# Performance work log

Measured on AMD Instinct MI355X. Metric: run time of the kernel, lower is better.

## Reference

```python
import jax, jax.numpy as jnp
import numpy as np

DIM, HEADS, EMB = 768, 16, 1024
DH = DIM // HEADS                 # 48, divisible by 3 for 3D RoPE
T, RES = 3, 24
KT, KH, KW = 3, 5, 5              # neighborhood kernel
MLP = 4 * DIM
EPS = 1e-5


def _ln(x, w=None, b=None):
    m = x.mean(-1, keepdims=True)
    v = x.var(-1, keepdims=True)
    y = (x - m) * jax.lax.rsqrt(v + EPS)
    if w is not None:
        y = y * w + b
    return y


def _rope_cos_sin():
    # 3D axial RoPE: dim_head split into 3 equal chunks (t, h, w axes)
    da = DH // 3
    half = da // 2
    inv = 1.0 / (10000.0 ** (jnp.arange(half, dtype=jnp.float32) * 2.0 / da))
    def ang(n):
        return jnp.arange(n, dtype=jnp.float32)[:, None] * inv[None, :]  # (n, half)
    at, ah, aw = ang(T), ang(RES), ang(RES)
    A = jnp.concatenate([
        jnp.broadcast_to(at[:, None, None, :], (T, RES, RES, half)),
        jnp.broadcast_to(ah[None, :, None, :], (T, RES, RES, half)),
        jnp.broadcast_to(aw[None, None, :, :], (T, RES, RES, half)),
    ], axis=-1).reshape(T * RES * RES, DH // 2)
    return jnp.cos(A), jnp.sin(A)


def _rope(x, cos, sin):  # x: (B, nh, THW, DH); interleaved pair rotation
    x1, x2 = x[..., 0::2], x[..., 1::2]
    o1 = x1 * cos - x2 * sin
    o2 = x1 * sin + x2 * cos
    return jnp.stack([o1, o2], axis=-1).reshape(x.shape)


def _nbr(n, k):
    # NATTEN window: centered, shifted inward at borders (always exactly k neighbors)
    start = jnp.clip(jnp.arange(n) - k // 2, 0, n - k)
    return start[:, None] + jnp.arange(k)  # (n, k)


def setup_inputs():
    key = jax.random.key(0)
    ks = jax.random.split(key, 8)
    r = lambda k, s: jax.random.normal(k, s, dtype=jnp.float32) * 0.02
    return {
        "x": jax.random.normal(ks[0], (T, DIM, RES, RES), dtype=jnp.float32),
        "emb": jax.random.normal(ks[1], (T, EMB), dtype=jnp.float32),
        "w_mod": r(ks[2], (EMB, 2 * DIM)),
        "b_mod": jnp.zeros((2 * DIM,), jnp.float32),
        "qn_w": jnp.ones((DH,), jnp.float32),
        "qn_b": jnp.zeros((DH,), jnp.float32),
        "kn_w": jnp.ones((DH,), jnp.float32),
        "kn_b": jnp.zeros((DH,), jnp.float32),
        "W_fused": r(ks[3], (DIM, 3 * DIM + MLP)),
        "b_fused": jnp.zeros((3 * DIM + MLP,), jnp.float32),
        "W_out": r(ks[4], (DIM, DIM)),
        "W_mlp": r(ks[5], (MLP, DIM)),
        "b_mlp": jnp.zeros((DIM,), jnp.float32),
    }


def reference(x, emb, w_mod, b_mod, qn_w, qn_b, kn_w, kn_b,
              W_fused, b_fused, W_out, W_mlp, b_mlp):
    B = x.shape[0] // T
    H = W = RES
    THW = T * H * W
    x5 = x.reshape(B, T, DIM, H, W)
    skip = jnp.transpose(x5, (0, 1, 3, 4, 2))          # (B,T,H,W,C)
    xf = skip.reshape(B, THW, DIM)
    # conditioning emb repeated over spatial positions
    embr = jnp.repeat(emb.reshape(B, T, EMB)[:, :, None, :], H * W, axis=2)
    embr = embr.reshape(B, THW, EMB)
    # NormalizeWithCond: LayerNorm (no affine) + AdaLN modulation from emb
    mod = jax.nn.silu(embr) @ w_mod + b_mod
    scale, shift = jnp.split(mod, 2, axis=-1)
    h = _ln(xf) * (1.0 + scale) + shift
    # fused QKV + MLP projection
    fused = h @ W_fused + b_fused
    qkv, mlp_h = fused[..., :3 * DIM], fused[..., 3 * DIM:]
    qkv = qkv.reshape(B, THW, 3, HEADS, DH).transpose(2, 0, 3, 1, 4)  # (3,B,nh,THW,d)
    q, k, v = qkv[0], qkv[1], qkv[2]
    q = _ln(q, qn_w, qn_b)
    k = _ln(k, kn_w, kn_b)
    cos, sin = _rope_cos_sin()
    q = _rope(q, cos, sin)
    k = _rope(k, cos, sin)
    q = q.reshape(B, HEADS, T, H, W, DH) * (DH ** -0.5)
    k = k.reshape(B, HEADS, T, H, W, DH)
    v = v.reshape(B, HEADS, T, H, W, DH)
    it, ih, iw = _nbr(T, KT), _nbr(H, KH), _nbr(W, KW)
    def gather(z):  # -> (B,nh,T,KT,H,KH,W,KW,d)
        return z[:, :, it][:, :, :, :, ih][:, :, :, :, :, :, iw]
    kg, vg = gather(k), gather(v)
    attn = jnp.einsum('bnthwd,bntahcwed->bnthwace', q, kg)
    attn = jax.nn.softmax(attn.reshape(B, HEADS, T, H, W, KT * KH * KW), axis=-1)
    attn = attn.reshape(B, HEADS, T, H, W, KT, KH, KW)
    xa = jnp.einsum('bnthwace,bntahcwed->bnthwd', attn, vg)
    xa = jnp.transpose(xa, (0, 2, 3, 4, 1, 5)).reshape(B, T, H, W, DIM)
    y = skip + xa @ W_out
    y = y.reshape(B, THW, DIM) + (jax.nn.silu(mlp_h) @ W_mlp + b_mlp)
    y = jnp.transpose(y.reshape(B, T, H, W, DIM), (0, 1, 4, 2, 3))
    return y.reshape(B * T, DIM, H, W)
```

## Files before the change

kernel.cpp:

```cpp
#include <hip/hip_runtime.h>
#include <hip/hip_bf16.h>
#include <math.h>

#define T_    3
#define RES_  24
#define DIM_  768
#define HEADS_ 16
#define DH_   48
#define EMB_  1024
#define HW_   576
#define THW_  1728
#define MP_   1792
#define MLP_  3072
#define NF_   5376
#define QKV_  2304
#define QK_   1536
#define KTOT_ 3840
#define SPLITK_ 6
#define EPS_  1e-5f

typedef __attribute__((ext_vector_type(8))) short bf16x8;
typedef __attribute__((ext_vector_type(4))) float f32x4;

__device__ __forceinline__ float siluf(float x) { return x / (1.f + expf(-x)); }

__device__ __forceinline__ unsigned short f2bf(float f) {
    __hip_bfloat16 b = __float2bfloat16(f);
    return *reinterpret_cast<unsigned short*>(&b);
}

__device__ __forceinline__ float bf2f(unsigned short u) {
    return __uint_as_float(((unsigned)u) << 16);
}

__device__ __forceinline__ void async_copy16(const void* g, void* l) {
    __builtin_amdgcn_global_load_lds(
        (__attribute__((address_space(1))) void*)g,
        (__attribute__((address_space(3))) void*)l,
        16, 0, 0);
}

__global__ __launch_bounds__(256) void prep_kernel(
    const float* __restrict__ W_fused, unsigned short* __restrict__ Bt1,
    const float* __restrict__ W_out, const float* __restrict__ W_mlp,
    unsigned short* __restrict__ Bt2,
    const float* __restrict__ emb, const float* __restrict__ w_mod,
    const float* __restrict__ b_mod, float* __restrict__ mod)
{
    __shared__ float buf[1152];
    int b = blockIdx.x;
    int tid = threadIdx.x;
    if (b < 4032) {
        float (*tile)[33] = (float(*)[33])buf;
        int n0 = (b % 168) * 32;
        int k0 = (b / 168) * 32;
        int c = tid & 31, r = tid >> 5;
#pragma unroll
        for (int i = 0; i < 4; ++i)
            tile[r + 8 * i][c] = W_fused[(size_t)(k0 + r + 8 * i) * NF_ + n0 + c];
        __syncthreads();
#pragma unroll
        for (int i = 0; i < 4; ++i)
            Bt1[(size_t)(n0 + r + 8 * i) * DIM_ + k0 + c] = f2bf(tile[c][r + 8 * i]);
    } else if (b < 6912) {
        int b2 = b - 4032;
        float (*tile)[33] = (float(*)[33])buf;
        int k0 = (b2 % 120) * 32;
        int n0 = (b2 / 120) * 32;
        int c = tid & 31, r = tid >> 5;
#pragma unroll
        for (int i = 0; i < 4; ++i) {
            int k = k0 + r + 8 * i;
            float v = (k < DIM_) ? W_out[(size_t)k * DIM_ + n0 + c]
                                 : W_mlp[(size_t)(k - DIM_) * DIM_ + n0 + c];
            tile[r + 8 * i][c] = v;
        }
        __syncthreads();
#pragma unroll
        for (int i = 0; i < 4; ++i)
            Bt2[(size_t)(n0 + r + 8 * i) * KTOT_ + k0 + c] = f2bf(tile[c][r + 8 * i]);
    } else {
        int b3 = b - 6912;
        int t = b3 / 12;
        int chunk = b3 - t * 12;
        float* se = buf;
        float* part = buf + 1024;
        for (int i = tid; i < EMB_; i += 256) {
            float e = emb[t * EMB_ + i];
            se[i] = e / (1.f + expf(-e));
        }
        __syncthreads();
        int r = tid >> 7;
        int c = tid & 127;
        int j = chunk * 128 + c;
        const float* wp = w_mod + j;
        float acc = 0.f;
        for (int e = r * 512; e < r * 512 + 512; ++e)
            acc += se[e] * wp[e * 1536];
        if (r == 1) part[c] = acc;
        __syncthreads();
        if (r == 0)
            mod[t * 1536 + j] = acc + part[c] + b_mod[j];
    }
}

__global__ __launch_bounds__(256) void ln_mod_kernel(
    const float* __restrict__ x, const float* __restrict__ mod,
    unsigned short* __restrict__ h)
{
    int m0 = blockIdx.x * 4;
    int t = m0 / HW_;
    int hw0 = m0 - t * HW_;
    const float* xp = x + (size_t)t * DIM_ * HW_ + hw0;
    int tid = threadIdx.x;
    float4 X0 = *(const float4*)(xp + (size_t)tid * HW_);
    float4 X1 = *(const float4*)(xp + (size_t)(tid + 256) * HW_);
    float4 X2 = *(const float4*)(xp + (size_t)(tid + 512) * HW_);
    float4 sv, sqv;
    sv.x = X0.x + X1.x + X2.x;  sv.y = X0.y + X1.y + X2.y;
    sv.z = X0.z + X1.z + X2.z;  sv.w = X0.w + X1.w + X2.w;
    sqv.x = X0.x*X0.x + X1.x*X1.x + X2.x*X2.x;
    sqv.y = X0.y*X0.y + X1.y*X1.y + X2.y*X2.y;
    sqv.z = X0.z*X0.z + X1.z*X1.z + X2.z*X2.z;
    sqv.w = X0.w*X0.w + X1.w*X1.w + X2.w*X2.w;
#pragma unroll
    for (int off = 32; off > 0; off >>= 1) {
        sv.x += __shfl_xor(sv.x, off, 64);  sv.y += __shfl_xor(sv.y, off, 64);
        sv.z += __shfl_xor(sv.z, off, 64);  sv.w += __shfl_xor(sv.w, off, 64);
        sqv.x += __shfl_xor(sqv.x, off, 64); sqv.y += __shfl_xor(sqv.y, off, 64);
        sqv.z += __shfl_xor(sqv.z, off, 64); sqv.w += __shfl_xor(sqv.w, off, 64);
    }
    __shared__ float4 ssum[4], ssq[4];
    int lane = tid & 63, wid = tid >> 6;
    if (lane == 0) { ssum[wid] = sv; ssq[wid] = sqv; }
    __syncthreads();
    float mean[4], rs[4];
#pragma unroll
    for (int j = 0; j < 4; ++j) {
        float tot  = ((const float*)&ssum[0])[j] + ((const float*)&ssum[1])[j]
                   + ((const float*)&ssum[2])[j] + ((const float*)&ssum[3])[j];
        float totq = ((const float*)&ssq[0])[j] + ((const float*)&ssq[1])[j]
                   + ((const float*)&ssq[2])[j] + ((const float*)&ssq[3])[j];
        float mn = tot * (1.f / 768.f);
        float var = totq * (1.f / 768.f) - mn * mn;
        mean[j] = mn;
        rs[j] = rsqrtf(var + EPS_);
    }
    const float* sc = mod + t * 1536;
    const float* sh = sc + 768;
#pragma unroll
    for (int cc = 0; cc < 3; ++cc) {
        int c = tid + cc * 256;
        float4 X = (cc == 0) ? X0 : (cc == 1) ? X1 : X2;
        float scl = 1.f + sc[c];
        float shf = sh[c];
        const float* Xp = (const float*)&X;
#pragma unroll
        for (int j = 0; j < 4; ++j)
            h[(size_t)(m0 + j) * DIM_ + c] =
                f2bf((Xp[j] - mean[j]) * rs[j] * scl + shf);
    }
}

__global__ __launch_bounds__(256) void gemm1_kernel(
    const unsigned short* __restrict__ A,
    const unsigned short* __restrict__ Bt,
    const float* __restrict__ bias,
    unsigned short* __restrict__ qkvb,
    unsigned short* __restrict__ vb,
    unsigned short* __restrict__ A2)
{
    const int K = DIM_;
    const int NI = K / 32;
    __shared__ unsigned short As[2][128 * 32];
    __shared__ unsigned short Bs[2][64 * 32];
    int tid = threadIdx.x;
    int bm = blockIdx.y * 128;
    int bn = blockIdx.x * 64;
    int wave = tid >> 6, lane = tid & 63;
    int quad = lane >> 4, l16 = lane & 15;
    int wm = (wave & 1) * 64;
    int wn = (wave >> 1) * 32;
    f32x4 acc[4][2] = {};
    int arow0 = tid >> 2,             akoff0 = (tid & 3) * 8;
    int arow1 = (tid + 256) >> 2,     akoff1 = (tid & 3) * 8;
    int brow = tid >> 2,              bkoff = (tid & 3) * 8;
    const unsigned short* Ag0 = A + (size_t)(bm + arow0) * K + akoff0;
    const unsigned short* Ag1 = A + (size_t)(bm + arow1) * K + akoff1;
    const unsigned short* Bg  = Bt + (size_t)(bn + brow) * K + bkoff;
    int la0 = arow0 * 32 + akoff0;
    int la1 = arow1 * 32 + akoff1;
    int lb  = brow * 32 + bkoff;
    async_copy16(Ag0, &As[0][la0]);
    async_copy16(Ag1, &As[0][la1]);
    async_copy16(Bg,  &Bs[0][lb]);
    for (int i = 0; i < NI; ++i) {
        __syncthreads();
        if (i + 1 < NI) {
            int k0 = (i + 1) * 32;
            int b = (i + 1) & 1;
            async_copy16(Ag0 + k0, &As[b][la0]);
            async_copy16(Ag1 + k0, &As[b][la1]);
            async_copy16(Bg + k0,  &Bs[b][lb]);
        }
        int b = i & 1;
        bf16x8 af[4], bf[2];
#pragma unroll
        for (int mt = 0; mt < 4; ++mt)
            af[mt] = *(const bf16x8*)&As[b][(wm + mt * 16 + l16) * 32 + quad * 8];
#pragma unroll
        for (int nt = 0; nt < 2; ++nt)
            bf[nt] = *(const bf16x8*)&Bs[b][(wn + nt * 16 + l16) * 32 + quad * 8];
#pragma unroll
        for (int mt = 0; mt < 4; ++mt)
#pragma unroll
            for (int nt = 0; nt < 2; ++nt)
                acc[mt][nt] = __builtin_amdgcn_mfma_f32_16x16x32_bf16(
                    af[mt], bf[nt], acc[mt][nt], 0, 0, 0);
    }
#pragma unroll
    for (int mt = 0; mt < 4; ++mt) {
#pragma unroll
        for (int nt = 0; nt < 2; ++nt) {
            int gcol = bn + wn + nt * 16 + l16;
            float b = bias[gcol];
#pragma unroll
            for (int r = 0; r < 4; ++r) {
                int grow = bm + wm + mt * 16 + quad * 4 + r;
                if (grow < THW_) {
                    float v = acc[mt][nt][r] + b;
                    if (gcol < QK_)
                        qkvb[(size_t)grow * QK_ + gcol] = f2bf(v);
                    else if (gcol < QKV_)
                        vb[(size_t)grow * DIM_ + (gcol - QK_)] = f2bf(v);
                    else
                        A2[(size_t)grow * KTOT_ + (gcol - QKV_ + DIM_)] = f2bf(siluf(v));
                }
            }
        }
    }
}

__global__ __launch_bounds__(256) void qkln_rope_kernel(
    const unsigned short* __restrict__ qkv,
    const float* __restrict__ qn_w, const float* __restrict__ qn_b,
    const float* __restrict__ kn_w, const float* __restrict__ kn_b,
    unsigned short* __restrict__ qb, unsigned short* __restrict__ kb)
{
    int tid = threadIdx.x;
    int lane = tid & 63, wid = tid >> 6;
    int idx = blockIdx.x * 4 + wid;
    int head = idx / THW_;
    int m = idx - head * THW_;
    const unsigned short* fp = qkv + (size_t)m * QK_ + head * DH_;
    float qv = 0.f, kv = 0.f;
    if (lane < DH_) { qv = bf2f(fp[lane]); kv = bf2f(fp[768 + lane]); }
    float s = qv, sq = qv * qv, sk = kv, sqk = kv * kv;
#pragma unroll
    for (int off = 32; off > 0; off >>= 1) {
        s   += __shfl_xor(s, off, 64);
        sq  += __shfl_xor(sq, off, 64);
        sk  += __shfl_xor(sk, off, 64);
        sqk += __shfl_xor(sqk, off, 64);
    }
    float mq = s  * (1.f / 48.f), vq = sq  * (1.f / 48.f) - mq * mq;
    float mk = sk * (1.f / 48.f), vk = sqk * (1.f / 48.f) - mk * mk;
    float qn = 0.f, kn = 0.f;
    if (lane < DH_) {
        qn = (qv - mq) * rsqrtf(vq + EPS_) * qn_w[lane] + qn_b[lane];
        kn = (kv - mk) * rsqrtf(vk + EPS_) * kn_w[lane] + kn_b[lane];
    }
    int t = m / HW_; int hw = m - t * HW_;
    int hh = hw / RES_; int ww = hw - hh * RES_;
    int i = lane >> 1;
    int grp = i >> 3, j = i & 7;
    float pos = (grp == 0) ? (float)t : (grp == 1) ? (float)hh : (float)ww;
    float invf = exp2f(-1.6609640474436813f * (float)j);
    float ang = pos * invf;
    float cs = cosf(ang), sn = sinf(ang);
    float qp = __shfl_xor(qn, 1, 64);
    float kp = __shfl_xor(kn, 1, 64);
    float qo, ko;
    if ((lane & 1) == 0) { qo = qn * cs - qp * sn; ko = kn * cs - kp * sn; }
    else                 { qo = qp * sn + qn * cs; ko = kp * sn + kn * cs; }
    if (lane < DH_) {
        size_t o = ((size_t)head * THW_ + m) * DH_ + lane;
        qb[o] = f2bf(qo * 0.14433756729740643f);
        kb[o] = f2bf(ko);
    }
}

__global__ __launch_bounds__(256) void attn_kernel(
    const unsigned short* __restrict__ qb, const unsigned short* __restrict__ kb,
    const unsigned short* __restrict__ vb, unsigned short* __restrict__ A2)
{
    __shared__ unsigned short U[64 * 168];
    __shared__ unsigned short Vt[48 * 168];

    int tid = threadIdx.x;
    int lane = tid & 63, wave = tid >> 6;
    int quad = lane >> 4, l16 = lane & 15;

    int head = blockIdx.x / 27;
    int tile = blockIdx.x - head * 27;
    int tt = tile / 9;
    int sp = tile - tt * 9;
    int h0 = (sp / 3) * 8;
    int w0 = (sp - (sp / 3) * 3) * 8;
    int u0h = min(max(h0 - 2, 0), RES_ - 12);
    int u0w = min(max(w0 - 2, 0), RES_ - 12);

    const unsigned short* qbh = qb + (size_t)head * THW_ * DH_;
    const unsigned short* kbh = kb + (size_t)head * THW_ * DH_;
    const unsigned short* vbh = vb + head * DH_;

    for (int i = tid; i < 48 * 24; i += 256) {
        int r = i / 24;
        Vt[r * 168 + 144 + (i - r * 24)] = 0;
    }

    int qbase = wave * 16;
    bf16x8 qf0, qf1;
    {
        int g = qbase + l16;
        int qtok = tt * HW_ + (h0 + (g >> 3)) * RES_ + (w0 + (g & 7));
        const unsigned short* qp = qbh + (size_t)qtok * DH_;
        qf0 = *(const bf16x8*)(qp + quad * 8);
        if (quad < 2) qf1 = *(const bf16x8*)(qp + 32 + quad * 8);
        else {
#pragma unroll
            for (int i = 0; i < 8; ++i) qf1[i] = 0;
        }
    }

    int vmask[4];
#pragma unroll
    for (int r = 0; r < 4; ++r) {
        int g = qbase + quad * 4 + r;
        int qh = h0 + (g >> 3), qw = w0 + (g & 7);
        int hs = min(max(qh - 2, 0), RES_ - 5);
        int ws = min(max(qw - 2, 0), RES_ - 5);
        int vm = 0;
#pragma unroll
        for (int nt = 0; nt < 9; ++nt) {
            int kk = nt * 16 + l16;
            int hc = u0h + kk / 12;
            int wc = u0w + kk - (kk / 12) * 12;
            int ok = (hc >= hs) & (hc < hs + 5) & (wc >= ws) & (wc < ws + 5);
            vm |= ok << nt;
        }
        vmask[r] = vm;
    }

    float mrow[4] = {-1e30f, -1e30f, -1e30f, -1e30f};
    float lrow[4] = {};
    f32x4 Oacc[3] = {};
    ushort4 z4; z4.x = 0; z4.y = 0; z4.z = 0; z4.w = 0;

    for (int a = 0; a < T_; ++a) {
        for (int i = tid; i < 144 * 12; i += 256) {
            int kk = i / 12;
            int g = i - kk * 12;
            int hc = u0h + kk / 12;
            int wc = u0w + kk - (kk / 12) * 12;
            int tok = a * HW_ + hc * RES_ + wc;
            ushort4 k4 = *(const ushort4*)(kbh + (size_t)tok * DH_ + 4 * g);
            *(ushort4*)&U[kk * 72 + 4 * g] = k4;
            ushort4 v4 = *(const ushort4*)(vbh + (size_t)tok * DIM_ + 4 * g);
            Vt[(4 * g + 0) * 168 + kk] = v4.x;
            Vt[(4 * g + 1) * 168 + kk] = v4.y;
            Vt[(4 * g + 2) * 168 + kk] = v4.z;
            Vt[(4 * g + 3) * 168 + kk] = v4.w;
        }
        for (int i = tid; i < 144 * 6; i += 256) {
            int kk = i / 6;
            int g = i - kk * 6;
            *(ushort4*)&U[kk * 72 + 48 + 4 * g] = z4;
        }
        __syncthreads();

        f32x4 sc[9];
#pragma unroll
        for (int nt = 0; nt < 9; ++nt) {
            bf16x8 kf0 = *(const bf16x8*)&U[(nt * 16 + l16) * 72 + quad * 8];
            bf16x8 kf1 = *(const bf16x8*)&U[(nt * 16 + l16) * 72 + 32 + quad * 8];
            f32x4 z = {};
            z = __builtin_amdgcn_mfma_f32_16x16x32_bf16(qf0, kf0, z, 0, 0, 0);
            sc[nt] = __builtin_amdgcn_mfma_f32_16x16x32_bf16(qf1, kf1, z, 0, 0, 0);
        }
        __syncthreads();

        float rmax[4] = {-1e30f, -1e30f, -1e30f, -1e30f};
#pragma unroll
        for (int nt = 0; nt < 9; ++nt)
#pragma unroll
            for (int r = 0; r < 4; ++r) {
                float s = ((vmask[r] >> nt) & 1) ? sc[nt][r] : -1e30f;
                sc[nt][r] = s;
                rmax[r] = fmaxf(rmax[r], s);
            }
#pragma unroll
        for (int off = 1; off < 16; off <<= 1)
#pragma unroll
            for (int r = 0; r < 4; ++r)
                rmax[r] = fmaxf(rmax[r], __shfl_xor(rmax[r], off));
        float alpha[4], rsum[4] = {};
#pragma unroll
        for (int r = 0; r < 4; ++r) {
            float mn = fmaxf(mrow[r], rmax[r]);
            alpha[r] = expf(mrow[r] - mn);
            mrow[r] = mn;
        }
#pragma unroll
        for (int nt = 0; nt < 9; ++nt)
#pragma unroll
            for (int r = 0; r < 4; ++r) {
                float p = expf(sc[nt][r] - mrow[r]);
                rsum[r] += p;
                U[(qbase + quad * 4 + r) * 168 + nt * 16 + l16] = f2bf(p);
            }
        {
            int rr = lane >> 2, cc = (lane & 3) * 4;
            *(ushort4*)&U[(qbase + rr) * 168 + 144 + cc] = z4;
        }
#pragma unroll
        for (int off = 1; off < 16; off <<= 1)
#pragma unroll
            for (int r = 0; r < 4; ++r)
                rsum[r] += __shfl_xor(rsum[r], off);
#pragma unroll
        for (int r = 0; r < 4; ++r)
            lrow[r] = lrow[r] * alpha[r] + rsum[r];
#pragma unroll
        for (int vt = 0; vt < 3; ++vt)
#pragma unroll
            for (int r = 0; r < 4; ++r)
                Oacc[vt][r] *= alpha[r];

#pragma unroll
        for (int ks = 0; ks < 5; ++ks) {
            bf16x8 pf = *(const bf16x8*)&U[(qbase + l16) * 168 + ks * 32 + quad * 8];
#pragma unroll
            for (int vt = 0; vt < 3; ++vt) {
                bf16x8 vf = *(const bf16x8*)&Vt[(vt * 16 + l16) * 168 + ks * 32 + quad * 8];
                Oacc[vt] = __builtin_amdgcn_mfma_f32_16x16x32_bf16(pf, vf, Oacc[vt], 0, 0, 0);
            }
        }
        __syncthreads();
    }

#pragma unroll
    for (int r = 0; r < 4; ++r) {
        int g = qbase + quad * 4 + r;
        int m = tt * HW_ + (h0 + (g >> 3)) * RES_ + (w0 + (g & 7));
        float inv = 1.f / lrow[r];
#pragma unroll
        for (int vt = 0; vt < 3; ++vt) {
            int d = vt * 16 + l16;
            A2[(size_t)m * KTOT_ + head * DH_ + d] = f2bf(Oacc[vt][r] * inv);
        }
    }
}

__global__ __launch_bounds__(256) void gemm2_kernel(
    const unsigned short* __restrict__ A,
    const unsigned short* __restrict__ Bt,
    unsigned short* __restrict__ P)
{
    const int K = KTOT_;
    const int NI = (KTOT_ / SPLITK_) / 32;
    __shared__ unsigned short As[2][128 * 32];
    __shared__ unsigned short Bs[2][64 * 32];
    int tid = threadIdx.x;
    int bm = blockIdx.y * 128;
    int bn = blockIdx.x * 64;
    int ks = blockIdx.z * (KTOT_ / SPLITK_);
    int wave = tid >> 6, lane = tid & 63;
    int quad = lane >> 4, l16 = lane & 15;
    int wm = (wave & 1) * 64;
    int wn = (wave >> 1) * 32;
    f32x4 acc[4][2] = {};
    int arow0 = tid >> 2,         akoff0 = (tid & 3) * 8;
    int arow1 = (tid + 256) >> 2, akoff1 = (tid & 3) * 8;
    int brow = tid >> 2,          bkoff = (tid & 3) * 8;
    const unsigned short* Ag0 = A + (size_t)(bm + arow0) * K + akoff0 + ks;
    const unsigned short* Ag1 = A + (size_t)(bm + arow1) * K + akoff1 + ks;
    const unsigned short* Bg  = Bt + (size_t)(bn + brow) * K + bkoff + ks;
    int la0 = arow0 * 32 + akoff0;
    int la1 = arow1 * 32 + akoff1;
    int lb  = brow * 32 + bkoff;
    async_copy16(Ag0, &As[0][la0]);
    async_copy16(Ag1, &As[0][la1]);
    async_copy16(Bg,  &Bs[0][lb]);
    for (int i = 0; i < NI; ++i) {
        __syncthreads();
        if (i + 1 < NI) {
            int k0 = (i + 1) * 32;
            int b = (i + 1) & 1;
            async_copy16(Ag0 + k0, &As[b][la0]);
            async_copy16(Ag1 + k0, &As[b][la1]);
            async_copy16(Bg + k0,  &Bs[b][lb]);
        }
        int b = i & 1;
        bf16x8 af[4], bf[2];
#pragma unroll
        for (int mt = 0; mt < 4; ++mt)
            af[mt] = *(const bf16x8*)&As[b][(wm + mt * 16 + l16) * 32 + quad * 8];
#pragma unroll
        for (int nt = 0; nt < 2; ++nt)
            bf[nt] = *(const bf16x8*)&Bs[b][(wn + nt * 16 + l16) * 32 + quad * 8];
#pragma unroll
        for (int mt = 0; mt < 4; ++mt)
#pragma unroll
            for (int nt = 0; nt < 2; ++nt)
                acc[mt][nt] = __builtin_amdgcn_mfma_f32_16x16x32_bf16(
                    af[mt], bf[nt], acc[mt][nt], 0, 0, 0);
    }
    unsigned short* Pp = P + (size_t)blockIdx.z * MP_ * DIM_;
#pragma unroll
    for (int mt = 0; mt < 4; ++mt) {
#pragma unroll
        for (int nt = 0; nt < 2; ++nt) {
            int gcol = bn + wn + nt * 16 + l16;
#pragma unroll
            for (int r = 0; r < 4; ++r) {
                int grow = bm + wm + mt * 16 + quad * 4 + r;
                if (grow < THW_)
                    Pp[(size_t)grow * DIM_ + gcol] = f2bf(acc[mt][nt][r]);
            }
        }
    }
}

__global__ __launch_bounds__(256) void reduce_out_kernel(
    const unsigned short* __restrict__ P, const float* __restrict__ x,
    const float* __restrict__ b_mlp, float* __restrict__ out)
{
    __shared__ float tile[32][65];
    int bm = blockIdx.x * 64;
    int bn = blockIdx.y * 32;
    int tid = threadIdx.x;
    int t = bm / HW_;
    int hw0 = bm - t * HW_;
    for (int i = tid; i < 512; i += 256) {
        int ml = i >> 3;
        int n4 = (i & 7) * 4;
        float s0 = 0.f, s1 = 0.f, s2 = 0.f, s3 = 0.f;
#pragma unroll
        for (int sI = 0; sI < SPLITK_; ++sI) {
            const unsigned short* pp =
                P + ((size_t)sI * MP_ + bm + ml) * DIM_ + bn + n4;
            ushort4 u = *(const ushort4*)pp;
            s0 += bf2f(u.x); s1 += bf2f(u.y);
            s2 += bf2f(u.z); s3 += bf2f(u.w);
        }
        tile[n4 + 0][ml] = s0;
        tile[n4 + 1][ml] = s1;
        tile[n4 + 2][ml] = s2;
        tile[n4 + 3][ml] = s3;
    }
    __syncthreads();
    for (int i = tid; i < 512; i += 256) {
        int n = i >> 4;
        int ms = (i & 15) * 4;
        int gn = bn + n;
        size_t base = ((size_t)t * DIM_ + gn) * HW_ + hw0 + ms;
        float bv = b_mlp[gn];
        float4 xv = *(const float4*)(x + base);
        float4 o;
        o.x = xv.x + bv + tile[n][ms + 0];
        o.y = xv.y + bv + tile[n][ms + 1];
        o.z = xv.z + bv + tile[n][ms + 2];
        o.w = xv.w + bv + tile[n][ms + 3];
        *(float4*)(out + base) = o;
    }
}

extern "C" void kernel_launch(void* const* d_in, const int* in_sizes, int n_in,
                              void* d_out, int out_size, void* d_ws, size_t ws_size,
                              hipStream_t stream) {
    const float* x       = (const float*)d_in[0];
    const float* emb     = (const float*)d_in[1];
    const float* w_mod   = (const float*)d_in[2];
    const float* b_mod   = (const float*)d_in[3];
    const float* qn_w    = (const float*)d_in[4];
    const float* qn_b    = (const float*)d_in[5];
    const float* kn_w    = (const float*)d_in[6];
    const float* kn_b    = (const float*)d_in[7];
    const float* W_fused = (const float*)d_in[8];
    const float* b_fused = (const float*)d_in[9];
    const float* W_out   = (const float*)d_in[10];
    const float* W_mlp   = (const float*)d_in[11];
    const float* b_mlp   = (const float*)d_in[12];
    float* out = (float*)d_out;

    char* w = (char*)d_ws;
    float* mod = (float*)w;            w += (size_t)4608 * 4;
    unsigned short* qkv = (unsigned short*)w;  w += (size_t)THW_ * QK_ * 2;
    unsigned short* vb  = (unsigned short*)w;  w += (size_t)THW_ * DIM_ * 2;
    unsigned short* qb  = (unsigned short*)w;  w += (size_t)HEADS_ * THW_ * DH_ * 2;
    unsigned short* kb  = (unsigned short*)w;  w += (size_t)HEADS_ * THW_ * DH_ * 2;
    unsigned short* h   = (unsigned short*)w;  w += (size_t)MP_ * DIM_ * 2;
    unsigned short* A2  = (unsigned short*)w;  w += (size_t)MP_ * KTOT_ * 2;
    unsigned short* Bt1 = (unsigned short*)w;  w += (size_t)NF_ * DIM_ * 2;
    unsigned short* Bt2 = (unsigned short*)w;  w += (size_t)DIM_ * KTOT_ * 2;
    unsigned short* P   = (unsigned short*)w;  w += (size_t)SPLITK_ * MP_ * DIM_ * 2;

    prep_kernel<<<6948, 256, 0, stream>>>(W_fused, Bt1, W_out, W_mlp, Bt2,
                                          emb, w_mod, b_mod, mod);
    ln_mod_kernel<<<THW_ / 4, 256, 0, stream>>>(x, mod, h);
    gemm1_kernel<<<dim3(NF_ / 64, MP_ / 128), 256, 0, stream>>>(h, Bt1, b_fused, qkv, vb, A2);
    qkln_rope_kernel<<<(HEADS_ * THW_) / 4, 256, 0, stream>>>(qkv, qn_w, qn_b, kn_w, kn_b, qb, kb);
    attn_kernel<<<HEADS_ * 27, 256, 0, stream>>>(qb, kb, vb, A2);
    gemm2_kernel<<<dim3(DIM_ / 64, MP_ / 128, SPLITK_), 256, 0, stream>>>(A2, Bt2, P);
    reduce_out_kernel<<<dim3(THW_ / 64, DIM_ / 32), 256, 0, stream>>>(P, x, b_mlp, out);
}
```

Measured before the change: 231.6 us.

## Fuse split-K reduction into gemm2 via last-block counter; merge LN into prep

After: 384.2 us. 65.8% more time.

```diff
diff --git a/kernel.cpp b/kernel.cpp
--- a/kernel.cpp
+++ b/kernel.cpp
@@ -17,6 +17,7 @@
 #define QK_   1536
 #define KTOT_ 3840
 #define SPLITK_ 6
+#define NCNT_ 168
 #define EPS_  1e-5f
 
 typedef __attribute__((ext_vector_type(8))) short bf16x8;
@@ -40,14 +41,43 @@
         16, 0, 0);
 }
 
-__global__ __launch_bounds__(256) void prep_kernel(
+__global__ __launch_bounds__(256) void mod_kernel(
+    const float* __restrict__ emb, const float* __restrict__ w_mod,
+    const float* __restrict__ b_mod, float* __restrict__ mod,
+    int* __restrict__ cnt)
+{
+    int t = blockIdx.y;
+    int chunk = blockIdx.x;
+    __shared__ float se[EMB_];
+    __shared__ float part[128];
+    int tid = threadIdx.x;
+    if (blockIdx.x == 0 && blockIdx.y == 0 && tid < NCNT_) cnt[tid] = 0;
+    for (int i = tid; i < EMB_; i += 256) {
+        float e = emb[t * EMB_ + i];
+        se[i] = e / (1.f + expf(-e));
+    }
+    __syncthreads();
+    int r = tid >> 7;
+    int c = tid & 127;
+    int j = chunk * 128 + c;
+    const float* wp = w_mod + j;
+    float acc = 0.f;
+    for (int e = r * 512; e < r * 512 + 512; ++e)
+        acc += se[e] * wp[e * 1536];
+    if (r == 1) part[c] = acc;
+    __syncthreads();
+    if (r == 0)
+        mod[t * 1536 + j] = acc + part[c] + b_mod[j];
+}
+
+__global__ __launch_bounds__(256) void prep_ln_kernel(
     const float* __restrict__ W_fused, unsigned short* __restrict__ Bt1,
     const float* __restrict__ W_out, const float* __restrict__ W_mlp,
     unsigned short* __restrict__ Bt2,
-    const float* __restrict__ emb, const float* __restrict__ w_mod,
-    const float* __restrict__ b_mod, float* __restrict__ mod)
+    const float* __restrict__ x, const float* __restrict__ mod,
+    unsigned short* __restrict__ h)
 {
-    __shared__ float buf[1152];
+    __shared__ float buf[1122];
     int b = blockIdx.x;
     int tid = threadIdx.x;
     if (b < 4032) {
@@ -80,85 +110,59 @@
         for (int i = 0; i < 4; ++i)
             Bt2[(size_t)(n0 + r + 8 * i) * KTOT_ + k0 + c] = f2bf(tile[c][r + 8 * i]);
     } else {
-        int b3 = b - 6912;
-        int t = b3 / 12;
-        int chunk = b3 - t * 12;
-        float* se = buf;
-        float* part = buf + 1024;
-        for (int i = tid; i < EMB_; i += 256) {
-            float e = emb[t * EMB_ + i];
-            se[i] = e / (1.f + expf(-e));
-        }
-        __syncthreads();
-        int r = tid >> 7;
-        int c = tid & 127;
-        int j = chunk * 128 + c;
-        const float* wp = w_mod + j;
-        float acc = 0.f;
-        for (int e = r * 512; e < r * 512 + 512; ++e)
-            acc += se[e] * wp[e * 1536];
-        if (r == 1) part[c] = acc;
-        __syncthreads();
-        if (r == 0)
-            mod[t * 1536 + j] = acc + part[c] + b_mod[j];
-    }
-}
-
-__global__ __launch_bounds__(256) void ln_mod_kernel(
-    const float* __restrict__ x, const float* __restrict__ mod,
-    unsigned short* __restrict__ h)
-{
-    int m0 = blockIdx.x * 4;
-    int t = m0 / HW_;
-    int hw0 = m0 - t * HW_;
-    const float* xp = x + (size_t)t * DIM_ * HW_ + hw0;
-    int tid = threadIdx.x;
-    float4 X0 = *(const float4*)(xp + (size_t)tid * HW_);
-    float4 X1 = *(const float4*)(xp + (size_t)(tid + 256) * HW_);
-    float4 X2 = *(const float4*)(xp + (size_t)(tid + 512) * HW_);
-    float4 sv, sqv;
-    sv.x = X0.x + X1.x + X2.x;  sv.y = X0.y + X1.y + X2.y;
-    sv.z = X0.z + X1.z + X2.z;  sv.w = X0.w + X1.w + X2.w;
-    sqv.x = X0.x*X0.x + X1.x*X1.x + X2.x*X2.x;
-    sqv.y = X0.y*X0.y + X1.y*X1.y + X2.y*X2.y;
-    sqv.z = X0.z*X0.z + X1.z*X1.z + X2.z*X2.z;
-    sqv.w = X0.w*X0.w + X1.w*X1.w + X2.w*X2.w;
-#pragma unroll
-    for (int off = 32; off > 0; off >>= 1) {
-        sv.x += __shfl_xor(sv.x, off, 64);  sv.y += __shfl_xor(sv.y, off, 64);
-        sv.z += __shfl_xor(sv.z, off, 64);  sv.w += __shfl_xor(sv.w, off, 64);
-        sqv.x += __shfl_xor(sqv.x, off, 64); sqv.y += __shfl_xor(sqv.y, off, 64);
-        sqv.z += __shfl_xor(sqv.z, off, 64); sqv.w += __shfl_xor(sqv.w, off, 64);
-    }
-    __shared__ float4 ssum[4], ssq[4];
-    int lane = tid & 63, wid = tid >> 6;
-    if (lane == 0) { ssum[wid] = sv; ssq[wid] = sqv; }
-    __syncthreads();
-    float mean[4], rs[4];
-#pragma unroll
-    for (int j = 0; j < 4; ++j) {
-        float tot  = ((const float*)&ssum[0])[j] + ((const float*)&ssum[1])[j]
-                   + ((const float*)&ssum[2])[j] + ((const float*)&ssum[3])[j];
-        float totq = ((const float*)&ssq[0])[j] + ((const float*)&ssq[1])[j]
-                   + ((const float*)&ssq[2])[j] + ((const float*)&ssq[3])[j];
-        float mn = tot * (1.f / 768.f);
-        float var = totq * (1.f / 768.f) - mn * mn;
-        mean[j] = mn;
-        rs[j] = rsqrtf(var + EPS_);
-    }
-    const float* sc = mod + t * 1536;
-    const float* sh = sc + 768;
-#pragma unroll
-    for (int cc = 0; cc < 3; ++cc) {
-        int c = tid + cc * 256;
-        float4 X = (cc == 0) ? X0 : (cc == 1) ? X1 : X2;
-        float scl = 1.f + sc[c];
-        float shf = sh[c];
-        const float* Xp = (const float*)&X;
-#pragma unroll
-        for (int j = 0; j < 4; ++j)
-            h[(size_t)(m0 + j) * DIM_ + c] =
-                f2bf((Xp[j] - mean[j]) * rs[j] * scl + shf);
+        int m0 = (b - 6912) * 4;
+        int t = m0 / HW_;
+        int hw0 = m0 - t * HW_;
+        const float* xp = x + (size_t)t * DIM_ * HW_ + hw0;
+        float4 X0 = *(const float4*)(xp + (size_t)tid * HW_);
+        float4 X1 = *(const float4*)(xp + (size_t)(tid + 256) * HW_);
+        float4 X2 = *(const float4*)(xp + (size_t)(tid + 512) * HW_);
+        float4 sv, sqv;
+        sv.x = X0.x + X1.x + X2.x;  sv.y = X0.y + X1.y + X2.y;
+        sv.z = X0.z + X1.z + X2.z;  sv.w = X0.w + X1.w + X2.w;
+        sqv.x = X0.x*X0.x + X1.x*X1.x + X2.x*X2.x;
+        sqv.y = X0.y*X0.y + X1.y*X1.y + X2.y*X2.y;
+        sqv.z = X0.z*X0.z + X1.z*X1.z + X2.z*X2.z;
+        sqv.w = X0.w*X0.w + X1.w*X1.w + X2.w*X2.w;
+#pragma unroll
+        for (int off = 32; off > 0; off >>= 1) {
+            sv.x += __shfl_xor(sv.x, off, 64);  sv.y += __shfl_xor(sv.y, off, 64);
+            sv.z += __shfl_xor(sv.z, off, 64);  sv.w += __shfl_xor(sv.w, off, 64);
+            sqv.x += __shfl_xor(sqv.x, off, 64); sqv.y += __shfl_xor(sqv.y, off, 64);
+            sqv.z += __shfl_xor(sqv.z, off, 64); sqv.w += __shfl_xor(sqv.w, off, 64);
+        }
+        float* ssum = buf;
+        float* ssq  = buf + 16;
+        int lane = tid & 63, wid = tid >> 6;
+        if (lane == 0) {
+            *(float4*)&ssum[wid * 4] = sv;
+            *(float4*)&ssq[wid * 4] = sqv;
+        }
+        __syncthreads();
+        float mean[4], rs[4];
+#pragma unroll
+        for (int j = 0; j < 4; ++j) {
+            float tot  = ssum[j] + ssum[4 + j] + ssum[8 + j] + ssum[12 + j];
+            float totq = ssq[j] + ssq[4 + j] + ssq[8 + j] + ssq[12 + j];
+            float mn = tot * (1.f / 768.f);
+            float var = totq * (1.f / 768.f) - mn * mn;
+            mean[j] = mn;
+            rs[j] = rsqrtf(var + EPS_);
+        }
+        const float* sc = mod + t * 1536;
+        const float* sh = sc + 768;
+#pragma unroll
+        for (int cc = 0; cc < 3; ++cc) {
+            int c = tid + cc * 256;
+            float4 X = (cc == 0) ? X0 : (cc == 1) ? X1 : X2;
+            float scl = 1.f + sc[c];
+            float shf = sh[c];
+            const float* Xp = (const float*)&X;
+#pragma unroll
+            for (int j = 0; j < 4; ++j)
+                h[(size_t)(m0 + j) * DIM_ + c] =
+                    f2bf((Xp[j] - mean[j]) * rs[j] * scl + shf);
+        }
     }
 }
 
@@ -465,12 +469,16 @@
 __global__ __launch_bounds__(256) void gemm2_kernel(
     const unsigned short* __restrict__ A,
     const unsigned short* __restrict__ Bt,
-    unsigned short* __restrict__ P)
+    unsigned short* __restrict__ P,
+    const float* __restrict__ x, const float* __restrict__ b_mlp,
+    float* __restrict__ out, int* __restrict__ cnt)
 {
     const int K = KTOT_;
     const int NI = (KTOT_ / SPLITK_) / 32;
-    __shared__ unsigned short As[2][128 * 32];
-    __shared__ unsigned short Bs[2][64 * 32];
+    __shared__ __align__(16) unsigned short smem[12288];
+    unsigned short* As0 = smem;
+    unsigned short* Bs0 = smem + 8192;
+    __shared__ int done_flag;
     int tid = threadIdx.x;
     int bm = blockIdx.y * 128;
     int bn = blockIdx.x * 64;
@@ -489,26 +497,26 @@
     int la0 = arow0 * 32 + akoff0;
     int la1 = arow1 * 32 + akoff1;
     int lb  = brow * 32 + bkoff;
-    async_copy16(Ag0, &As[0][la0]);
-    async_copy16(Ag1, &As[0][la1]);
-    async_copy16(Bg,  &Bs[0][lb]);
+    async_copy16(Ag0, &As0[la0]);
+    async_copy16(Ag1, &As0[la1]);
+    async_copy16(Bg,  &Bs0[lb]);
     for (int i = 0; i < NI; ++i) {
         __syncthreads();
         if (i + 1 < NI) {
             int k0 = (i + 1) * 32;
             int b = (i + 1) & 1;
-            async_copy16(Ag0 + k0, &As[b][la0]);
-            async_copy16(Ag1 + k0, &As[b][la1]);
-            async_copy16(Bg + k0,  &Bs[b][lb]);
+            async_copy16(Ag0 + k0, &As0[b * 4096 + la0]);
+            async_copy16(Ag1 + k0, &As0[b * 4096 + la1]);
+            async_copy16(Bg + k0,  &Bs0[b * 2048 + lb]);
         }
         int b = i & 1;
         bf16x8 af[4], bf[2];
 #pragma unroll
         for (int mt = 0; mt < 4; ++mt)
-            af[mt] = *(const bf16x8*)&As[b][(wm + mt * 16 + l16) * 32 + quad * 8];
+            af[mt] = *(const bf16x8*)&As0[b * 4096 + (wm + mt * 16 + l16) * 32 + quad * 8];
 #pragma unroll
         for (int nt = 0; nt < 2; ++nt)
-            bf[nt] = *(const bf16x8*)&Bs[b][(wn + nt * 16 + l16) * 32 + quad * 8];
+            bf[nt] = *(const bf16x8*)&Bs0[b * 2048 + (wn + nt * 16 + l16) * 32 + quad * 8];
 #pragma unroll
         for (int mt = 0; mt < 4; ++mt)
 #pragma unroll
@@ -530,49 +538,53 @@
             }
         }
     }
-}
-
-__global__ __launch_bounds__(256) void reduce_out_kernel(
-    const unsigned short* __restrict__ P, const float* __restrict__ x,
-    const float* __restrict__ b_mlp, float* __restrict__ out)
-{
-    __shared__ float tile[32][65];
-    int bm = blockIdx.x * 64;
-    int bn = blockIdx.y * 32;
-    int tid = threadIdx.x;
-    int t = bm / HW_;
-    int hw0 = bm - t * HW_;
-    for (int i = tid; i < 512; i += 256) {
-        int ml = i >> 3;
-        int n4 = (i & 7) * 4;
-        float s0 = 0.f, s1 = 0.f, s2 = 0.f, s3 = 0.f;
-#pragma unroll
-        for (int sI = 0; sI < SPLITK_; ++sI) {
-            const unsigned short* pp =
-                P + ((size_t)sI * MP_ + bm + ml) * DIM_ + bn + n4;
-            ushort4 u = *(const ushort4*)pp;
-            s0 += bf2f(u.x); s1 += bf2f(u.y);
-            s2 += bf2f(u.z); s3 += bf2f(u.w);
-        }
-        tile[n4 + 0][ml] = s0;
-        tile[n4 + 1][ml] = s1;
-        tile[n4 + 2][ml] = s2;
-        tile[n4 + 3][ml] = s3;
-    }
+    __threadfence();
     __syncthreads();
-    for (int i = tid; i < 512; i += 256) {
-        int n = i >> 4;
-        int ms = (i & 15) * 4;
-        int gn = bn + n;
-        size_t base = ((size_t)t * DIM_ + gn) * HW_ + hw0 + ms;
-        float bv = b_mlp[gn];
-        float4 xv = *(const float4*)(x + base);
-        float4 o;
-        o.x = xv.x + bv + tile[n][ms + 0];
-        o.y = xv.y + bv + tile[n][ms + 1];
-        o.z = xv.z + bv + tile[n][ms + 2];
-        o.w = xv.w + bv + tile[n][ms + 3];
-        *(float4*)(out + base) = o;
+    if (tid == 0)
+        done_flag = atomicAdd(&cnt[blockIdx.y * 12 + blockIdx.x], 1);
+    __syncthreads();
+    if (done_flag != SPLITK_ - 1) return;
+    __threadfence();
+    float (*rt)[65] = (float(*)[65])smem;
+    for (int sub = 0; sub < 4; ++sub) {
+        int m0 = bm + (sub >> 1) * 64;
+        int n0 = bn + (sub & 1) * 32;
+        if (m0 >= THW_) break;
+        int t = m0 / HW_;
+        int hw0 = m0 - t * HW_;
+        for (int i = tid; i < 512; i += 256) {
+            int ml = i >> 3;
+            int n4 = (i & 7) * 4;
+            float s0 = 0.f, s1 = 0.f, s2 = 0.f, s3 = 0.f;
+#pragma unroll
+            for (int sI = 0; sI < SPLITK_; ++sI) {
+                const unsigned short* pp =
+                    P + ((size_t)sI * MP_ + m0 + ml) * DIM_ + n0 + n4;
+                ushort4 u = *(const ushort4*)pp;
+                s0 += bf2f(u.x); s1 += bf2f(u.y);
+                s2 += bf2f(u.z); s3 += bf2f(u.w);
+            }
+            rt[n4 + 0][ml] = s0;
+            rt[n4 + 1][ml] = s1;
+            rt[n4 + 2][ml] = s2;
+            rt[n4 + 3][ml] = s3;
+        }
+        __syncthreads();
+        for (int i = tid; i < 512; i += 256) {
+            int n = i >> 4;
+            int ms = (i & 15) * 4;
+            int gn = n0 + n;
+            size_t base = ((size_t)t * DIM_ + gn) * HW_ + hw0 + ms;
+            float bv = b_mlp[gn];
+            float4 xv = *(const float4*)(x + base);
+            float4 o;
+            o.x = xv.x + bv + rt[n][ms + 0];
+            o.y = xv.y + bv + rt[n][ms + 1];
+            o.z = xv.z + bv + rt[n][ms + 2];
+            o.w = xv.w + bv + rt[n][ms + 3];
+            *(float4*)(out + base) = o;
+        }
+        __syncthreads();
     }
 }
 
@@ -605,13 +617,14 @@
     unsigned short* Bt1 = (unsigned short*)w;  w += (size_t)NF_ * DIM_ * 2;
     unsigned short* Bt2 = (unsigned short*)w;  w += (size_t)DIM_ * KTOT_ * 2;
     unsigned short* P   = (unsigned short*)w;  w += (size_t)SPLITK_ * MP_ * DIM_ * 2;
-
-    prep_kernel<<<6948, 256, 0, stream>>>(W_fused, Bt1, W_out, W_mlp, Bt2,
-                                          emb, w_mod, b_mod, mod);
-    ln_mod_kernel<<<THW_ / 4, 256, 0, stream>>>(x, mod, h);
+    int* cnt            = (int*)w;             w += (size_t)NCNT_ * 4;
+
+    mod_kernel<<<dim3(12, 3), 256, 0, stream>>>(emb, w_mod, b_mod, mod, cnt);
+    prep_ln_kernel<<<7344, 256, 0, stream>>>(W_fused, Bt1, W_out, W_mlp, Bt2,
+                                             x, mod, h);
     gemm1_kernel<<<dim3(NF_ / 64, MP_ / 128), 256, 0, stream>>>(h, Bt1, b_fused, qkv, vb, A2);
     qkln_rope_kernel<<<(HEADS_ * THW_) / 4, 256, 0, stream>>>(qkv, qn_w, qn_b, kn_w, kn_b, qb, kb);
     attn_kernel<<<HEADS_ * 27, 256, 0, stream>>>(qb, kb, vb, A2);
-    gemm2_kernel<<<dim3(DIM_ / 64, MP_ / 128, SPLITK_), 256, 0, stream>>>(A2, Bt2, P);
-    reduce_out_kernel<<<dim3(THW_ / 64, DIM_ / 32), 256, 0, stream>>>(P, x, b_mlp, out);
-}
+    gemm2_kernel<<<dim3(DIM_ / 64, MP_ / 128, SPLITK_), 256, 0, stream>>>(
+        A2, Bt2, P, x, b_mlp, out, cnt);
+}
```
